# Kernel optimization log

Measured on AMD Instinct MI355X. Metric: run time of the kernel, lower is better.

## Reference

```python
import jax, jax.numpy as jnp
import numpy as np

B, T, C = 32, 128, 64
E, H = 8, 4            # feat_dim, num_heads
D = E // H             # head_dim = 2
HID = 32               # hidden_dim


def setup_inputs() -> dict:
    key = jax.random.key(0)
    ks = jax.random.split(key, 20)
    s = 0.1
    return {
        "x": jax.random.normal(ks[0], (B, T, C), jnp.float32),
        # input_proj: Linear(C, C)
        "W_in": jax.random.normal(ks[1], (C, C), jnp.float32) * s,
        "b_in": jax.random.normal(ks[2], (C,), jnp.float32) * s,
        # time_step_score: Linear(C, C//4) -> GELU -> Linear(C//4, 1) -> Sigmoid
        "W_ts1": jax.random.normal(ks[3], (C // 4, C), jnp.float32) * s,
        "b_ts1": jax.random.normal(ks[4], (C // 4,), jnp.float32) * s,
        "W_ts2": jax.random.normal(ks[5], (1, C // 4), jnp.float32) * s,
        "b_ts2": jax.random.normal(ks[6], (1,), jnp.float32) * s,
        # per-channel GRU(1 -> E): torch gate order (r, z, n)
        "W_ih": jax.random.normal(ks[7], (C, 3 * E), jnp.float32) * s,      # input size 1
        "W_hh": jax.random.normal(ks[8], (C, 3 * E, E), jnp.float32) * s,
        "b_ih": jax.random.normal(ks[9], (C, 3 * E), jnp.float32) * s,
        "b_hh": jax.random.normal(ks[10], (C, 3 * E), jnp.float32) * s,
        # shared MultiheadAttention(E, 4): packed in_proj + out_proj
        "W_qkv": jax.random.normal(ks[11], (3 * E, E), jnp.float32) * s,
        "b_qkv": jax.random.normal(ks[12], (3 * E,), jnp.float32) * s,
        "W_o": jax.random.normal(ks[13], (E, E), jnp.float32) * s,
        "b_o": jax.random.normal(ks[14], (E,), jnp.float32) * s,
        # out_proj: Linear(C*E, HID)
        "W_out": jax.random.normal(ks[15], (HID, C * E), jnp.float32) * s,
        "b_out": jax.random.normal(ks[16], (HID,), jnp.float32) * s,
    }


def _forward(x, W_in, b_in, W_ts1, b_ts1, W_ts2, b_ts2,
             W_ih, W_hh, b_ih, b_hh, W_qkv, b_qkv, W_o, b_o, W_out, b_out):
    bs, ts, c = x.shape
    # time step importance: per-timestep MLP over the raw features
    h1 = jax.nn.gelu(jnp.einsum('btc,fc->btf', x, W_ts1) + b_ts1, approximate=False)
    ts_imp = jax.nn.sigmoid(jnp.einsum('btf,of->bto', h1, W_ts2) + b_ts2)[..., 0]  # [B,T]

    xp = jnp.einsum('btc,dc->btd', x, W_in) + b_in  # [B,T,C]

    # Batched per-channel GRU scan over time. state h: [B,C,E]
    def step(h, x_t):
        gi = x_t[:, :, None] * W_ih[None] + b_ih          # [B,C,3E]
        gh = jnp.einsum('bce,cge->bcg', h, W_hh) + b_hh   # [B,C,3E]
        ir, iz, inn = gi[..., :E], gi[..., E:2 * E], gi[..., 2 * E:]
        hr, hz, hn = gh[..., :E], gh[..., E:2 * E], gh[..., 2 * E:]
        r = jax.nn.sigmoid(ir + hr)
        z = jax.nn.sigmoid(iz + hz)
        n = jnp.tanh(inn + r * hn)
        h_new = (1.0 - z) * n + z * h
        return h_new, h_new

    h0 = jnp.zeros((bs, c, E), xp.dtype)
    _, hs = jax.lax.scan(step, h0, jnp.transpose(xp, (1, 0, 2)))  # [T,B,C,E]
    hs_bcte = jnp.transpose(hs, (1, 2, 0, 3))                     # [B,C,T,E]

    # Shared MHA applied independently per channel (batched over B*C)
    qkv = jnp.einsum('bcte,fe->bctf', hs_bcte, W_qkv) + b_qkv     # [B,C,T,3E]
    q, k, v = qkv[..., :E], qkv[..., E:2 * E], qkv[..., 2 * E:]
    def heads(t):
        return t.reshape(bs, c, ts, H, D)
    q, k, v = heads(q), heads(k), heads(v)
    scores = jnp.einsum('bcthd,bcshd->bchts', q, k) / np.sqrt(D)
    attn = jax.nn.softmax(scores, axis=-1)
    o = jnp.einsum('bchts,bcshd->bcthd', attn, v).reshape(bs, c, ts, E)
    attn_out = jnp.einsum('bcte,fe->bctf', o, W_o) + b_o          # [B,C,T,E]
    attention = jnp.transpose(attn_out, (0, 2, 1, 3))             # [B,T,C,E]

    out_flat = jnp.transpose(hs, (1, 0, 2, 3)).reshape(bs, ts, c * E)  # [B,T,C*E]
    out = jnp.einsum('btf,hf->bth', out_flat, W_out) + b_out           # [B,T,HID]

    feat_imp = jax.nn.sigmoid(attention.sum(axis=(1, 3)))   # [B,C]
    tsf_imp = jax.nn.sigmoid(attention.sum(axis=-1))        # [B,T,C]
    return out[:, -1, :], feat_imp, ts_imp, tsf_imp


def reference(x, W_in, b_in, W_ts1, b_ts1, W_ts2, b_ts2,
              W_ih, W_hh, b_ih, b_hh, W_qkv, b_qkv, W_o, b_o, W_out, b_out):
    return _forward(x, W_in, b_in, W_ts1, b_ts1, W_ts2, b_ts2,
                    W_ih, W_hh, b_ih, b_hh, W_qkv, b_qkv, W_o, b_o, W_out, b_out)
```

## Files before the change

kernel.cpp:

```cpp
#include <hip/hip_runtime.h>
#include <hip/hip_bf16.h>
#include <math.h>

#define B_ 32
#define T_ 128
#define C_ 64
#define E_ 8
#define HID_ 32

#define LOG2E 1.44269504088896341f

__device__ __forceinline__ float fast_rcp(float x) { return __builtin_amdgcn_rcpf(x); }
__device__ __forceinline__ float fast_sigmoid(float x) {
    return fast_rcp(1.0f + exp2f(-LOG2E * x));
}
__device__ __forceinline__ float fast_tanh(float x) {
    float xc = __builtin_amdgcn_fmed3f(x, -15.0f, 15.0f);
    float t = exp2f(2.0f * LOG2E * xc);
    return (t - 1.0f) * fast_rcp(t + 1.0f);
}

__global__ __launch_bounds__(64) void k_gru(
    const float* __restrict__ x, const float* __restrict__ W_in, const float* __restrict__ b_in,
    const float* __restrict__ W_ih, const float* __restrict__ W_hh,
    const float* __restrict__ b_ih, const float* __restrict__ b_hh,
    float* __restrict__ hs, float* __restrict__ fh)
{
    const int tid = threadIdx.x;
    const int ci = tid >> 3;
    const int e = tid & 7;
    const int chain = blockIdx.x * 8 + ci;
    const int b = chain >> 6;
    const int c = chain & 63;

    __shared__ float wsh[8][C_];
    __shared__ float xc[8][T_ + 1];

#pragma unroll
    for (int i = 0; i < 8; ++i) {
        int idx = tid * 8 + i;
        int ci2 = idx >> 6;
        int cc = (blockIdx.x * 8 + ci2) & 63;
        wsh[ci2][idx & 63] = W_in[cc * C_ + (idx & 63)];
    }
    __syncthreads();

    const float bi = b_in[c];
    for (int tt = 0; tt < 16; ++tt) {
        const int t = e * 16 + tt;
        const float4* xr = (const float4*)(x + (b * T_ + t) * C_);
        float a = bi;
#pragma unroll
        for (int k4 = 0; k4 < 16; ++k4) {
            float4 xv = xr[k4];
            a = fmaf(xv.x, wsh[ci][k4 * 4 + 0], a);
            a = fmaf(xv.y, wsh[ci][k4 * 4 + 1], a);
            a = fmaf(xv.z, wsh[ci][k4 * 4 + 2], a);
            a = fmaf(xv.w, wsh[ci][k4 * 4 + 3], a);
        }
        xc[ci][t] = a;
    }
    __syncthreads();

    float wr[E_], wz[E_], wn[E_];
#pragma unroll
    for (int j = 0; j < E_; ++j) {
        wr[j] = W_hh[(c * 24 + 0 * E_ + e) * E_ + j];
        wz[j] = W_hh[(c * 24 + 1 * E_ + e) * E_ + j];
        wn[j] = W_hh[(c * 24 + 2 * E_ + e) * E_ + j];
    }
    const float wir = W_ih[c * 24 + e], wiz = W_ih[c * 24 + E_ + e], win = W_ih[c * 24 + 2 * E_ + e];
    const float cr = b_ih[c * 24 + e] + b_hh[c * 24 + e];
    const float cz = b_ih[c * 24 + E_ + e] + b_hh[c * 24 + E_ + e];
    const float bin_ = b_ih[c * 24 + 2 * E_ + e];
    const float bhn  = b_hh[c * 24 + 2 * E_ + e];

    float h = 0.0f;
    float xv = xc[ci][0];
    float* ho = hs + (size_t)chain * T_ * E_ + e;
    for (int t = 0; t < T_; ++t) {
        float xvn = xc[ci][t + 1];
        float hj0 = __shfl(h, 0, 8), hj1 = __shfl(h, 1, 8);
        float hj2 = __shfl(h, 2, 8), hj3 = __shfl(h, 3, 8);
        float hj4 = __shfl(h, 4, 8), hj5 = __shfl(h, 5, 8);
        float hj6 = __shfl(h, 6, 8), hj7 = __shfl(h, 7, 8);
        float grx = fmaf(xv, wir, cr);
        float gzx = fmaf(xv, wiz, cz);
        float gnx = fmaf(xv, win, bin_);
        float r0 = fmaf(hj1, wr[1], hj0 * wr[0]);
        float r1 = fmaf(hj3, wr[3], hj2 * wr[2]);
        float r2 = fmaf(hj5, wr[5], hj4 * wr[4]);
        float r3 = fmaf(hj7, wr[7], hj6 * wr[6]);
        float z0 = fmaf(hj1, wz[1], hj0 * wz[0]);
        float z1 = fmaf(hj3, wz[3], hj2 * wz[2]);
        float z2 = fmaf(hj5, wz[5], hj4 * wz[4]);
        float z3 = fmaf(hj7, wz[7], hj6 * wz[6]);
        float n0 = fmaf(hj1, wn[1], hj0 * wn[0]);
        float n1 = fmaf(hj3, wn[3], hj2 * wn[2]);
        float n2 = fmaf(hj5, wn[5], hj4 * wn[4]);
        float n3 = fmaf(hj7, wn[7], hj6 * wn[6]);
        float gr = grx + ((r0 + r1) + (r2 + r3));
        float gz = gzx + ((z0 + z1) + (z2 + z3));
        float hn = bhn + ((n0 + n1) + (n2 + n3));
        float r = fast_sigmoid(gr);
        float z = fast_sigmoid(gz);
        float nn = fast_tanh(fmaf(r, hn, gnx));
        h = fmaf(z, h - nn, nn);
        ho[t * E_] = h;
        xv = xvn;
    }
    fh[chain * E_ + e] = h;
}

__global__ __launch_bounds__(256) void k_attn(
    const float* __restrict__ hs, const float* __restrict__ W_qkv, const float* __restrict__ b_qkv,
    const float* __restrict__ W_o, const float* __restrict__ b_o,
    float* __restrict__ feat_imp, float* __restrict__ tsf_imp)
{
    const int bc = blockIdx.x;
    const int b = bc >> 6, c = bc & 63;
    const int tid = threadIdx.x;
    const int t2 = tid & 63;
    const int sq = tid >> 6;

    __shared__ __align__(16) float ks[T_][E_];
    __shared__ __align__(16) float us[T_][4];
    __shared__ float qsT[E_][T_];
    __shared__ float pacc[3][T_][8];
    __shared__ float red[T_];

    const float qscale = 0.70710678118654752f * LOG2E;

    {
        const int row = (tid < 128) ? tid : (tid - 128);
        const float4* hp = (const float4*)(hs + (size_t)bc * T_ * E_ + row * E_);
        float4 h0 = hp[0], h1 = hp[1];
        float hr[E_] = {h0.x, h0.y, h0.z, h0.w, h1.x, h1.y, h1.z, h1.w};
        if (tid < 128) {
            float kv[E_];
#pragma unroll
            for (int f = 0; f < E_; ++f) {
                float a = b_qkv[E_ + f];
#pragma unroll
                for (int j = 0; j < E_; ++j) a = fmaf(hr[j], W_qkv[(E_ + f) * E_ + j], a);
                kv[f] = a;
            }
            ((float4*)&ks[row][0])[0] = make_float4(kv[0], kv[1], kv[2], kv[3]);
            ((float4*)&ks[row][0])[1] = make_float4(kv[4], kv[5], kv[6], kv[7]);
#pragma unroll
            for (int f = 0; f < E_; ++f) {
                float a = b_qkv[f];
#pragma unroll
                for (int j = 0; j < E_; ++j) a = fmaf(hr[j], W_qkv[f * E_ + j], a);
                qsT[f][row] = a * qscale;
            }
        } else {
            float ws[E_];
#pragma unroll
            for (int d = 0; d < E_; ++d) {
                float w = 0.0f;
#pragma unroll
                for (int fp = 0; fp < E_; ++fp) w += W_o[fp * E_ + d];
                ws[d] = w;
            }
            float vv[E_];
#pragma unroll
            for (int f = 0; f < E_; ++f) {
                float a = b_qkv[2 * E_ + f];
#pragma unroll
                for (int j = 0; j < E_; ++j) a = fmaf(hr[j], W_qkv[(2 * E_ + f) * E_ + j], a);
                vv[f] = a;
            }
            float4 uu;
            uu.x = fmaf(vv[1], ws[1], vv[0] * ws[0]);
            uu.y = fmaf(vv[3], ws[3], vv[2] * ws[2]);
            uu.z = fmaf(vv[5], ws[5], vv[4] * ws[4]);
            uu.w = fmaf(vv[7], ws[7], vv[6] * ws[6]);
            *((float4*)&us[row][0]) = uu;
        }
    }
    __syncthreads();

    float q0[E_], q1[E_];
#pragma unroll
    for (int f = 0; f < E_; ++f) { q0[f] = qsT[f][t2]; q1[f] = qsT[f][t2 + 64]; }

    float l0[4] = {0.f,0.f,0.f,0.f}, S0[4] = {0.f,0.f,0.f,0.f};
    float l1[4] = {0.f,0.f,0.f,0.f}, S1[4] = {0.f,0.f,0.f,0.f};
    const float* kb = &ks[sq * 32][0];
    const float* ub = &us[sq * 32][0];
#pragma unroll 8
    for (int i = 0; i < 32; ++i) {
        float4 k0 = *(const float4*)(kb + i * 8);
        float4 k1 = *(const float4*)(kb + i * 8 + 4);
        float4 uu = *(const float4*)(ub + i * 4);
        float p00 = exp2f(fmaf(q0[1], k0.y, q0[0] * k0.x));
        float p01 = exp2f(fmaf(q0[3], k0.w, q0[2] * k0.z));
        float p02 = exp2f(fmaf(q0[5], k1.y, q0[4] * k1.x));
        float p03 = exp2f(fmaf(q0[7], k1.w, q0[6] * k1.z));
        float p10 = exp2f(fmaf(q1[1], k0.y, q1[0] * k0.x));
        float p11 = exp2f(fmaf(q1[3], k0.w, q1[2] * k0.z));
        float p12 = exp2f(fmaf(q1[5], k1.y, q1[4] * k1.x));
        float p13 = exp2f(fmaf(q1[7], k1.w, q1[6] * k1.z));
        l0[0] += p00; l0[1] += p01; l0[2] += p02; l0[3] += p03;
        l1[0] += p10; l1[1] += p11; l1[2] += p12; l1[3] += p13;
        S0[0] = fmaf(p00, uu.x, S0[0]); S0[1] = fmaf(p01, uu.y, S0[1]);
        S0[2] = fmaf(p02, uu.z, S0[2]); S0[3] = fmaf(p03, uu.w, S0[3]);
        S1[0] = fmaf(p10, uu.x, S1[0]); S1[1] = fmaf(p11, uu.y, S1[1]);
        S1[2] = fmaf(p12, uu.z, S1[2]); S1[3] = fmaf(p13, uu.w, S1[3]);
    }

    if (sq > 0) {
        float* pr = &pacc[sq - 1][t2][0];
#pragma unroll
        for (int i = 0; i < 4; ++i) { pr[i] = l0[i]; pr[4 + i] = S0[i]; }
        pr = &pacc[sq - 1][t2 + 64][0];
#pragma unroll
        for (int i = 0; i < 4; ++i) { pr[i] = l1[i]; pr[4 + i] = S1[i]; }
    }
    __syncthreads();

    if (sq == 0) {
        float bsum = 0.0f;
#pragma unroll
        for (int fp = 0; fp < E_; ++fp) bsum += b_o[fp];
#pragma unroll
        for (int qq = 0; qq < 3; ++qq) {
#pragma unroll
            for (int i = 0; i < 4; ++i) {
                l0[i] += pacc[qq][t2][i];       S0[i] += pacc[qq][t2][4 + i];
                l1[i] += pacc[qq][t2 + 64][i];  S1[i] += pacc[qq][t2 + 64][4 + i];
            }
        }
        float Sa = bsum, Sb = bsum;
#pragma unroll
        for (int hh = 0; hh < 4; ++hh) {
            Sa = fmaf(S0[hh], fast_rcp(l0[hh]), Sa);
            Sb = fmaf(S1[hh], fast_rcp(l1[hh]), Sb);
        }
        tsf_imp[(size_t)b * T_ * C_ + (size_t)t2 * C_ + c] = fast_sigmoid(Sa);
        tsf_imp[(size_t)b * T_ * C_ + (size_t)(t2 + 64) * C_ + c] = fast_sigmoid(Sb);
        red[t2] = Sa;
        red[t2 + 64] = Sb;
    }
    __syncthreads();
    for (int off = 64; off > 0; off >>= 1) {
        if (tid < off) red[tid] += red[tid + off];
        __syncthreads();
    }
    if (tid == 0) feat_imp[bc] = fast_sigmoid(red[0]);
}

__global__ __launch_bounds__(64) void k_ts(
    const float* __restrict__ x,
    const float* __restrict__ W_ts1, const float* __restrict__ b_ts1,
    const float* __restrict__ W_ts2, const float* __restrict__ b_ts2,
    float* __restrict__ ts_imp)
{
    const int bt = blockIdx.x;
    const int tid = threadIdx.x;
    __shared__ float xs[C_];
    __shared__ float h1[16];
    xs[tid] = x[bt * C_ + tid];
    __syncthreads();
    if (tid < 16) {
        float a = b_ts1[tid];
#pragma unroll
        for (int k = 0; k < C_; ++k) a = fmaf(xs[k], W_ts1[tid * C_ + k], a);
        h1[tid] = 0.5f * a * (1.0f + erff(a * 0.70710678118654752f));
    }
    __syncthreads();
    if (tid == 0) {
        float s = b_ts2[0];
#pragma unroll
        for (int k = 0; k < 16; ++k) s = fmaf(h1[k], W_ts2[k], s);
        ts_imp[bt] = fast_sigmoid(s);
    }
}

__global__ __launch_bounds__(64) void k_out(
    const float* __restrict__ fh, const float* __restrict__ W_out, const float* __restrict__ b_out,
    float* __restrict__ out0)
{
    const int b = blockIdx.x;
    const int tid = threadIdx.x;
    __shared__ float hf[C_ * E_];
    const float4* src = (const float4*)(fh + (b * C_ + tid) * E_);
    float4* dst = (float4*)(hf + tid * E_);
    dst[0] = src[0];
    dst[1] = src[1];
    __syncthreads();
    if (tid < HID_) {
        float a = b_out[tid];
        const float* wo = W_out + tid * (C_ * E_);
        for (int k = 0; k < C_ * E_; ++k) a = fmaf(hf[k], wo[k], a);
        out0[b * HID_ + tid] = a;
    }
}

extern "C" void kernel_launch(void* const* d_in, const int* in_sizes, int n_in,
                              void* d_out, int out_size, void* d_ws, size_t ws_size,
                              hipStream_t stream) {
    (void)in_sizes; (void)n_in; (void)out_size; (void)ws_size;

    float* out0 = (float*)d_out;
    float* feat = out0 + B_ * HID_;
    float* tsim = feat + B_ * C_;
    float* tsf  = tsim + B_ * T_;

    const float* x     = (const float*)d_in[0];
    const float* W_in  = (const float*)d_in[1];
    const float* b_in  = (const float*)d_in[2];
    const float* W_ts1 = (const float*)d_in[3];
    const float* b_ts1 = (const float*)d_in[4];
    const float* W_ts2 = (const float*)d_in[5];
    const float* b_ts2 = (const float*)d_in[6];
    const float* W_ih  = (const float*)d_in[7];
    const float* W_hh  = (const float*)d_in[8];
    const float* b_ih  = (const float*)d_in[9];
    const float* b_hh  = (const float*)d_in[10];
    const float* W_qkv = (const float*)d_in[11];
    const float* b_qkv = (const float*)d_in[12];
    const float* W_o   = (const float*)d_in[13];
    const float* b_o   = (const float*)d_in[14];
    const float* W_out = (const float*)d_in[15];
    const float* b_out = (const float*)d_in[16];

    float* fhb = (float*)d_ws;
    float* hsb = fhb + B_ * C_ * E_;

    hipLaunchKernelGGL(k_gru, dim3(B_ * C_ / 8), dim3(64), 0, stream,
                       x, W_in, b_in, W_ih, W_hh, b_ih, b_hh, hsb, fhb);
    hipLaunchKernelGGL(k_attn, dim3(B_ * C_), dim3(256), 0, stream,
                       hsb, W_qkv, b_qkv, W_o, b_o, feat, tsf);
    hipLaunchKernelGGL(k_ts, dim3(B_ * T_), dim3(64), 0, stream,
                       x, W_ts1, b_ts1, W_ts2, b_ts2, tsim);
    hipLaunchKernelGGL(k_out, dim3(B_), dim3(64), 0, stream,
                       fhb, W_out, b_out, out0);
}
```

Before: 93.19 us.

## Merge four kernels into two, stage GRU outputs in LDS, restructure attention reduction

Folds the time-step MLP into extra blocks of the GRU kernel and the final output projection into an extra block of the attention kernel, so the launch sequence shrinks from four kernels to two. GRU hidden states are buffered in shared memory and written back as coalesced float4 stores instead of strided scalar stores. The attention inner loop now gives each query row to a lane pair, which combine partial sums by shuffle, replacing the cross-wave LDS partial-accumulation pass and the tree reduction. Raw hardware exp2 builtins replace exp2f. The tradeoffs are a larger LDS footprint in the GRU kernel and a single output-projection block that may run as a serial tail.

```diff
diff --git a/kernel.cpp b/kernel.cpp
--- a/kernel.cpp
+++ b/kernel.cpp
@@ -11,30 +11,61 @@
 #define LOG2E 1.44269504088896341f
 
 __device__ __forceinline__ float fast_rcp(float x) { return __builtin_amdgcn_rcpf(x); }
+#if __has_builtin(__builtin_amdgcn_exp2f)
+__device__ __forceinline__ float fast_exp2(float x) { return __builtin_amdgcn_exp2f(x); }
+#else
+__device__ __forceinline__ float fast_exp2(float x) { return exp2f(x); }
+#endif
 __device__ __forceinline__ float fast_sigmoid(float x) {
-    return fast_rcp(1.0f + exp2f(-LOG2E * x));
+    return fast_rcp(1.0f + fast_exp2(-LOG2E * x));
 }
 __device__ __forceinline__ float fast_tanh(float x) {
     float xc = __builtin_amdgcn_fmed3f(x, -15.0f, 15.0f);
-    float t = exp2f(2.0f * LOG2E * xc);
+    float t = fast_exp2(2.0f * LOG2E * xc);
     return (t - 1.0f) * fast_rcp(t + 1.0f);
 }
 
-__global__ __launch_bounds__(64) void k_gru(
+__global__ __launch_bounds__(64) void k_gru_ts(
     const float* __restrict__ x, const float* __restrict__ W_in, const float* __restrict__ b_in,
     const float* __restrict__ W_ih, const float* __restrict__ W_hh,
     const float* __restrict__ b_ih, const float* __restrict__ b_hh,
-    float* __restrict__ hs, float* __restrict__ fh)
+    const float* __restrict__ W_ts1, const float* __restrict__ b_ts1,
+    const float* __restrict__ W_ts2, const float* __restrict__ b_ts2,
+    float* __restrict__ hs, float* __restrict__ fh, float* __restrict__ ts_imp)
 {
     const int tid = threadIdx.x;
+
+    __shared__ float wsh[8][C_];
+    __shared__ float xc[8][T_ + 1];
+    __shared__ float hsb[T_][68];
+
+    if (blockIdx.x >= 256) {
+        const int bt = blockIdx.x - 256;
+        float* xs = &wsh[0][0];
+        float* h1 = &xc[0][0];
+        xs[tid] = x[bt * C_ + tid];
+        __syncthreads();
+        if (tid < 16) {
+            float a = b_ts1[tid];
+#pragma unroll
+            for (int k = 0; k < C_; ++k) a = fmaf(xs[k], W_ts1[tid * C_ + k], a);
+            h1[tid] = 0.5f * a * (1.0f + erff(a * 0.70710678118654752f));
+        }
+        __syncthreads();
+        if (tid == 0) {
+            float s = b_ts2[0];
+#pragma unroll
+            for (int k = 0; k < 16; ++k) s = fmaf(h1[k], W_ts2[k], s);
+            ts_imp[bt] = fast_sigmoid(s);
+        }
+        return;
+    }
+
     const int ci = tid >> 3;
     const int e = tid & 7;
     const int chain = blockIdx.x * 8 + ci;
     const int b = chain >> 6;
     const int c = chain & 63;
-
-    __shared__ float wsh[8][C_];
-    __shared__ float xc[8][T_ + 1];
 
 #pragma unroll
     for (int i = 0; i < 8; ++i) {
@@ -77,7 +108,6 @@
 
     float h = 0.0f;
     float xv = xc[ci][0];
-    float* ho = hs + (size_t)chain * T_ * E_ + e;
     for (int t = 0; t < T_; ++t) {
         float xvn = xc[ci][t + 1];
         float hj0 = __shfl(h, 0, 8), hj1 = __shfl(h, 1, 8);
@@ -106,34 +136,68 @@
         float z = fast_sigmoid(gz);
         float nn = fast_tanh(fmaf(r, hn, gnx));
         h = fmaf(z, h - nn, nn);
-        ho[t * E_] = h;
+        hsb[t][tid] = h;
         xv = xvn;
     }
     fh[chain * E_ + e] = h;
-}
-
-__global__ __launch_bounds__(256) void k_attn(
+    __syncthreads();
+
+    float4* gdst = (float4*)(hs + (size_t)blockIdx.x * 8 * T_ * E_);
+#pragma unroll
+    for (int k = 0; k < 32; ++k) {
+        int idx4 = k * 64 + tid;
+        int fi = idx4 * 4;
+        int cc = fi >> 10;
+        int t = (fi >> 3) & 127;
+        int ee = fi & 7;
+        gdst[idx4] = *(const float4*)&hsb[t][cc * 8 + ee];
+    }
+}
+
+__global__ __launch_bounds__(256) void k_attn_out(
     const float* __restrict__ hs, const float* __restrict__ W_qkv, const float* __restrict__ b_qkv,
     const float* __restrict__ W_o, const float* __restrict__ b_o,
-    float* __restrict__ feat_imp, float* __restrict__ tsf_imp)
+    const float* __restrict__ fh, const float* __restrict__ W_out, const float* __restrict__ b_out,
+    float* __restrict__ out0, float* __restrict__ feat_imp, float* __restrict__ tsf_imp)
 {
+    const int tid = threadIdx.x;
+
+    if (blockIdx.x == B_ * C_) {
+#pragma unroll
+        for (int pi = tid; pi < B_ * HID_; pi += 256) {
+            int bb = pi >> 5, o = pi & 31;
+            const float4* hv = (const float4*)(fh + bb * C_ * E_);
+            const float4* wv = (const float4*)(W_out + o * C_ * E_);
+            float a = b_out[o];
+#pragma unroll 16
+            for (int k4 = 0; k4 < 128; ++k4) {
+                float4 h4 = hv[k4], w4 = wv[k4];
+                a = fmaf(h4.x, w4.x, a); a = fmaf(h4.y, w4.y, a);
+                a = fmaf(h4.z, w4.z, a); a = fmaf(h4.w, w4.w, a);
+            }
+            out0[pi] = a;
+        }
+        return;
+    }
+
     const int bc = blockIdx.x;
     const int b = bc >> 6, c = bc & 63;
-    const int tid = threadIdx.x;
-    const int t2 = tid & 63;
-    const int sq = tid >> 6;
+    const int w = tid >> 6;
+    const int lane = tid & 63;
+    const int ri = lane >> 1;
+    const int sh = lane & 1;
+    const int row = w * 32 + ri;
 
     __shared__ __align__(16) float ks[T_][E_];
     __shared__ __align__(16) float us[T_][4];
     __shared__ float qsT[E_][T_];
-    __shared__ float pacc[3][T_][8];
-    __shared__ float red[T_];
+    __shared__ float red4[4];
 
     const float qscale = 0.70710678118654752f * LOG2E;
 
     {
-        const int row = (tid < 128) ? tid : (tid - 128);
-        const float4* hp = (const float4*)(hs + (size_t)bc * T_ * E_ + row * E_);
+        const int srow = (tid < 128) ? tid : (tid - 128);
+        const float4* hp = (const float4*)(hs + (size_t)bc * T_ * E_ + srow * E_);
         float4 h0 = hp[0], h1 = hp[1];
         float hr[E_] = {h0.x, h0.y, h0.z, h0.w, h1.x, h1.y, h1.z, h1.w};
         if (tid < 128) {
@@ -145,23 +209,23 @@
                 for (int j = 0; j < E_; ++j) a = fmaf(hr[j], W_qkv[(E_ + f) * E_ + j], a);
                 kv[f] = a;
             }
-            ((float4*)&ks[row][0])[0] = make_float4(kv[0], kv[1], kv[2], kv[3]);
-            ((float4*)&ks[row][0])[1] = make_float4(kv[4], kv[5], kv[6], kv[7]);
+            ((float4*)&ks[srow][0])[0] = make_float4(kv[0], kv[1], kv[2], kv[3]);
+            ((float4*)&ks[srow][0])[1] = make_float4(kv[4], kv[5], kv[6], kv[7]);
 #pragma unroll
             for (int f = 0; f < E_; ++f) {
                 float a = b_qkv[f];
 #pragma unroll
                 for (int j = 0; j < E_; ++j) a = fmaf(hr[j], W_qkv[f * E_ + j], a);
-                qsT[f][row] = a * qscale;
+                qsT[f][srow] = a * qscale;
             }
         } else {
             float ws[E_];
 #pragma unroll
             for (int d = 0; d < E_; ++d) {
-                float w = 0.0f;
-#pragma unroll
-                for (int fp = 0; fp < E_; ++fp) w += W_o[fp * E_ + d];
-                ws[d] = w;
+                float wv = 0.0f;
+#pragma unroll
+                for (int fp = 0; fp < E_; ++fp) wv += W_o[fp * E_ + d];
+                ws[d] = wv;
             }
             float vv[E_];
 #pragma unroll
@@ -176,126 +240,58 @@
             uu.y = fmaf(vv[3], ws[3], vv[2] * ws[2]);
             uu.z = fmaf(vv[5], ws[5], vv[4] * ws[4]);
             uu.w = fmaf(vv[7], ws[7], vv[6] * ws[6]);
-            *((float4*)&us[row][0]) = uu;
-        }
-    }
-    __syncthreads();
-
-    float q0[E_], q1[E_];
-#pragma unroll
-    for (int f = 0; f < E_; ++f) { q0[f] = qsT[f][t2]; q1[f] = qsT[f][t2 + 64]; }
-
-    float l0[4] = {0.f,0.f,0.f,0.f}, S0[4] = {0.f,0.f,0.f,0.f};
-    float l1[4] = {0.f,0.f,0.f,0.f}, S1[4] = {0.f,0.f,0.f,0.f};
-    const float* kb = &ks[sq * 32][0];
-    const float* ub = &us[sq * 32][0];
+            *((float4*)&us[srow][0]) = uu;
+        }
+    }
+    __syncthreads();
+
+    float q[E_];
+#pragma unroll
+    for (int f = 0; f < E_; ++f) q[f] = qsT[f][row];
+
+    float l[4] = {0.f, 0.f, 0.f, 0.f};
+    float S[4] = {0.f, 0.f, 0.f, 0.f};
+    const float* kb = &ks[sh * 64][0];
+    const float* ub = &us[sh * 64][0];
 #pragma unroll 8
-    for (int i = 0; i < 32; ++i) {
+    for (int i = 0; i < 64; ++i) {
         float4 k0 = *(const float4*)(kb + i * 8);
         float4 k1 = *(const float4*)(kb + i * 8 + 4);
         float4 uu = *(const float4*)(ub + i * 4);
-        float p00 = exp2f(fmaf(q0[1], k0.y, q0[0] * k0.x));
-        float p01 = exp2f(fmaf(q0[3], k0.w, q0[2] * k0.z));
-        float p02 = exp2f(fmaf(q0[5], k1.y, q0[4] * k1.x));
-        float p03 = exp2f(fmaf(q0[7], k1.w, q0[6] * k1.z));
-        float p10 = exp2f(fmaf(q1[1], k0.y, q1[0] * k0.x));
-        float p11 = exp2f(fmaf(q1[3], k0.w, q1[2] * k0.z));
-        float p12 = exp2f(fmaf(q1[5], k1.y, q1[4] * k1.x));
-        float p13 = exp2f(fmaf(q1[7], k1.w, q1[6] * k1.z));
-        l0[0] += p00; l0[1] += p01; l0[2] += p02; l0[3] += p03;
-        l1[0] += p10; l1[1] += p11; l1[2] += p12; l1[3] += p13;
-        S0[0] = fmaf(p00, uu.x, S0[0]); S0[1] = fmaf(p01, uu.y, S0[1]);
-        S0[2] = fmaf(p02, uu.z, S0[2]); S0[3] = fmaf(p03, uu.w, S0[3]);
-        S1[0] = fmaf(p10, uu.x, S1[0]); S1[1] = fmaf(p11, uu.y, S1[1]);
-        S1[2] = fmaf(p12, uu.z, S1[2]); S1[3] = fmaf(p13, uu.w, S1[3]);
-    }
-
-    if (sq > 0) {
-        float* pr = &pacc[sq - 1][t2][0];
-#pragma unroll
-        for (int i = 0; i < 4; ++i) { pr[i] = l0[i]; pr[4 + i] = S0[i]; }
-        pr = &pacc[sq - 1][t2 + 64][0];
-#pragma unroll
-        for (int i = 0; i < 4; ++i) { pr[i] = l1[i]; pr[4 + i] = S1[i]; }
-    }
-    __syncthreads();
-
-    if (sq == 0) {
-        float bsum = 0.0f;
-#pragma unroll
-        for (int fp = 0; fp < E_; ++fp) bsum += b_o[fp];
-#pragma unroll
-        for (int qq = 0; qq < 3; ++qq) {
-#pragma unroll
-            for (int i = 0; i < 4; ++i) {
-                l0[i] += pacc[qq][t2][i];       S0[i] += pacc[qq][t2][4 + i];
-                l1[i] += pacc[qq][t2 + 64][i];  S1[i] += pacc[qq][t2 + 64][4 + i];
-            }
-        }
-        float Sa = bsum, Sb = bsum;
-#pragma unroll
-        for (int hh = 0; hh < 4; ++hh) {
-            Sa = fmaf(S0[hh], fast_rcp(l0[hh]), Sa);
-            Sb = fmaf(S1[hh], fast_rcp(l1[hh]), Sb);
-        }
-        tsf_imp[(size_t)b * T_ * C_ + (size_t)t2 * C_ + c] = fast_sigmoid(Sa);
-        tsf_imp[(size_t)b * T_ * C_ + (size_t)(t2 + 64) * C_ + c] = fast_sigmoid(Sb);
-        red[t2] = Sa;
-        red[t2 + 64] = Sb;
-    }
-    __syncthreads();
-    for (int off = 64; off > 0; off >>= 1) {
-        if (tid < off) red[tid] += red[tid + off];
-        __syncthreads();
-    }
-    if (tid == 0) feat_imp[bc] = fast_sigmoid(red[0]);
-}
-
-__global__ __launch_bounds__(64) void k_ts(
-    const float* __restrict__ x,
-    const float* __restrict__ W_ts1, const float* __restrict__ b_ts1,
-    const float* __restrict__ W_ts2, const float* __restrict__ b_ts2,
-    float* __restrict__ ts_imp)
-{
-    const int bt = blockIdx.x;
-    const int tid = threadIdx.x;
-    __shared__ float xs[C_];
-    __shared__ float h1[16];
-    xs[tid] = x[bt * C_ + tid];
-    __syncthreads();
-    if (tid < 16) {
-        float a = b_ts1[tid];
-#pragma unroll
-        for (int k = 0; k < C_; ++k) a = fmaf(xs[k], W_ts1[tid * C_ + k], a);
-        h1[tid] = 0.5f * a * (1.0f + erff(a * 0.70710678118654752f));
-    }
-    __syncthreads();
-    if (tid == 0) {
-        float s = b_ts2[0];
-#pragma unroll
-        for (int k = 0; k < 16; ++k) s = fmaf(h1[k], W_ts2[k], s);
-        ts_imp[bt] = fast_sigmoid(s);
-    }
-}
-
-__global__ __launch_bounds__(64) void k_out(
-    const float* __restrict__ fh, const float* __restrict__ W_out, const float* __restrict__ b_out,
-    float* __restrict__ out0)
-{
-    const int b = blockIdx.x;
-    const int tid = threadIdx.x;
-    __shared__ float hf[C_ * E_];
-    const float4* src = (const float4*)(fh + (b * C_ + tid) * E_);
-    float4* dst = (float4*)(hf + tid * E_);
-    dst[0] = src[0];
-    dst[1] = src[1];
-    __syncthreads();
-    if (tid < HID_) {
-        float a = b_out[tid];
-        const float* wo = W_out + tid * (C_ * E_);
-        for (int k = 0; k < C_ * E_; ++k) a = fmaf(hf[k], wo[k], a);
-        out0[b * HID_ + tid] = a;
-    }
+        float p0 = fast_exp2(fmaf(q[1], k0.y, q[0] * k0.x));
+        float p1 = fast_exp2(fmaf(q[3], k0.w, q[2] * k0.z));
+        float p2 = fast_exp2(fmaf(q[5], k1.y, q[4] * k1.x));
+        float p3 = fast_exp2(fmaf(q[7], k1.w, q[6] * k1.z));
+        l[0] += p0; l[1] += p1; l[2] += p2; l[3] += p3;
+        S[0] = fmaf(p0, uu.x, S[0]);
+        S[1] = fmaf(p1, uu.y, S[1]);
+        S[2] = fmaf(p2, uu.z, S[2]);
+        S[3] = fmaf(p3, uu.w, S[3]);
+    }
+
+#pragma unroll
+    for (int i = 0; i < 4; ++i) {
+        l[i] += __shfl_xor(l[i], 1);
+        S[i] += __shfl_xor(S[i], 1);
+    }
+
+    float bsum = 0.0f;
+#pragma unroll
+    for (int fp = 0; fp < E_; ++fp) bsum += b_o[fp];
+    float Sv = bsum;
+#pragma unroll
+    for (int hh = 0; hh < 4; ++hh) Sv = fmaf(S[hh], fast_rcp(l[hh]), Sv);
+
+    if (sh == 0)
+        tsf_imp[(size_t)b * T_ * C_ + (size_t)row * C_ + c] = fast_sigmoid(Sv);
+
+    float fsum = Sv;
+#pragma unroll
+    for (int off = 2; off <= 32; off <<= 1) fsum += __shfl_xor(fsum, off);
+    if (lane == 0) red4[w] = fsum;
+    __syncthreads();
+    if (tid == 0)
+        feat_imp[bc] = fast_sigmoid(red4[0] + red4[1] + red4[2] + red4[3]);
 }
 
 extern "C" void kernel_launch(void* const* d_in, const int* in_sizes, int n_in,
@@ -329,12 +325,10 @@
     float* fhb = (float*)d_ws;
     float* hsb = fhb + B_ * C_ * E_;
 
-    hipLaunchKernelGGL(k_gru, dim3(B_ * C_ / 8), dim3(64), 0, stream,
-                       x, W_in, b_in, W_ih, W_hh, b_ih, b_hh, hsb, fhb);
-    hipLaunchKernelGGL(k_attn, dim3(B_ * C_), dim3(256), 0, stream,
-                       hsb, W_qkv, b_qkv, W_o, b_o, feat, tsf);
-    hipLaunchKernelGGL(k_ts, dim3(B_ * T_), dim3(64), 0, stream,
-                       x, W_ts1, b_ts1, W_ts2, b_ts2, tsim);
-    hipLaunchKernelGGL(k_out, dim3(B_), dim3(64), 0, stream,
-                       fhb, W_out, b_out, out0);
-}
+    hipLaunchKernelGGL(k_gru_ts, dim3(256 + B_ * T_), dim3(64), 0, stream,
+                       x, W_in, b_in, W_ih, W_hh, b_ih, b_hh,
+                       W_ts1, b_ts1, W_ts2, b_ts2, hsb, fhb, tsim);
+    hipLaunchKernelGGL(k_attn_out, dim3(B_ * C_ + 1), dim3(256), 0, stream,
+                       hsb, W_qkv, b_qkv, W_o, b_o,
+                       fhb, W_out, b_out, out0, feat, tsf);
+}
```

Measured after the change: 126.7 us. +35.9%, slower.

## Split input projection into separate kernel and give each GRU thread two hidden units

Applied to the files above, without the earlier changes.

Moves the input projection out of the GRU kernel into a new k_pre kernel that writes xp to workspace, so the GRU kernel only loads precomputed values into shared memory. The GRU is remapped from 8 threads per chain (one hidden unit each) to 4 threads per chain (two units each), which replaces the 8 broadcast shuffles with a few xor shuffles and permuted weights, and packs 16 chains into each block. This aims to shorten the serial recurrence step and cut the redundant projection work done in every GRU block. The cost is an extra kernel launch, a global round-trip for xp, and half as many GRU blocks, which lowers parallelism.

```diff
diff --git a/kernel.cpp b/kernel.cpp
--- a/kernel.cpp
+++ b/kernel.cpp
@@ -11,105 +11,124 @@
 #define LOG2E 1.44269504088896341f
 
 __device__ __forceinline__ float fast_rcp(float x) { return __builtin_amdgcn_rcpf(x); }
+__device__ __forceinline__ float fast_exp2(float x) { return exp2f(x); }
 __device__ __forceinline__ float fast_sigmoid(float x) {
-    return fast_rcp(1.0f + exp2f(-LOG2E * x));
+    return fast_rcp(1.0f + fast_exp2(-LOG2E * x));
 }
 __device__ __forceinline__ float fast_tanh(float x) {
     float xc = __builtin_amdgcn_fmed3f(x, -15.0f, 15.0f);
-    float t = exp2f(2.0f * LOG2E * xc);
+    float t = fast_exp2(2.0f * LOG2E * xc);
     return (t - 1.0f) * fast_rcp(t + 1.0f);
 }
 
+__global__ __launch_bounds__(64) void k_pre(
+    const float* __restrict__ x, const float* __restrict__ W_in, const float* __restrict__ b_in,
+    float* __restrict__ xp)
+{
+    const int bt = blockIdx.x;
+    const int tid = threadIdx.x;
+    __shared__ __align__(16) float4 xs4[16];
+    if (tid < 16) xs4[tid] = ((const float4*)(x + bt * C_))[tid];
+    __syncthreads();
+    float a = b_in[tid];
+    const float4* w4 = (const float4*)(W_in + tid * C_);
+#pragma unroll
+    for (int k4 = 0; k4 < 16; ++k4) {
+        float4 xv = xs4[k4];
+        float4 wv = w4[k4];
+        a = fmaf(xv.x, wv.x, a); a = fmaf(xv.y, wv.y, a);
+        a = fmaf(xv.z, wv.z, a); a = fmaf(xv.w, wv.w, a);
+    }
+    xp[bt * C_ + tid] = a;
+}
+
 __global__ __launch_bounds__(64) void k_gru(
-    const float* __restrict__ x, const float* __restrict__ W_in, const float* __restrict__ b_in,
-    const float* __restrict__ W_ih, const float* __restrict__ W_hh,
+    const float* __restrict__ xp, const float* __restrict__ W_ih, const float* __restrict__ W_hh,
     const float* __restrict__ b_ih, const float* __restrict__ b_hh,
     float* __restrict__ hs, float* __restrict__ fh)
 {
     const int tid = threadIdx.x;
-    const int ci = tid >> 3;
-    const int e = tid & 7;
-    const int chain = blockIdx.x * 8 + ci;
-    const int b = chain >> 6;
+    const int ci = tid >> 2;
+    const int q  = tid & 3;
+    const int chain = blockIdx.x * 16 + ci;
     const int c = chain & 63;
 
-    __shared__ float wsh[8][C_];
-    __shared__ float xc[8][T_ + 1];
-
-#pragma unroll
-    for (int i = 0; i < 8; ++i) {
-        int idx = tid * 8 + i;
-        int ci2 = idx >> 6;
-        int cc = (blockIdx.x * 8 + ci2) & 63;
-        wsh[ci2][idx & 63] = W_in[cc * C_ + (idx & 63)];
-    }
-    __syncthreads();
-
-    const float bi = b_in[c];
-    for (int tt = 0; tt < 16; ++tt) {
-        const int t = e * 16 + tt;
-        const float4* xr = (const float4*)(x + (b * T_ + t) * C_);
-        float a = bi;
-#pragma unroll
-        for (int k4 = 0; k4 < 16; ++k4) {
-            float4 xv = xr[k4];
-            a = fmaf(xv.x, wsh[ci][k4 * 4 + 0], a);
-            a = fmaf(xv.y, wsh[ci][k4 * 4 + 1], a);
-            a = fmaf(xv.z, wsh[ci][k4 * 4 + 2], a);
-            a = fmaf(xv.w, wsh[ci][k4 * 4 + 3], a);
-        }
-        xc[ci][t] = a;
-    }
-    __syncthreads();
-
-    float wr[E_], wz[E_], wn[E_];
-#pragma unroll
-    for (int j = 0; j < E_; ++j) {
-        wr[j] = W_hh[(c * 24 + 0 * E_ + e) * E_ + j];
-        wz[j] = W_hh[(c * 24 + 1 * E_ + e) * E_ + j];
-        wn[j] = W_hh[(c * 24 + 2 * E_ + e) * E_ + j];
-    }
-    const float wir = W_ih[c * 24 + e], wiz = W_ih[c * 24 + E_ + e], win = W_ih[c * 24 + 2 * E_ + e];
-    const float cr = b_ih[c * 24 + e] + b_hh[c * 24 + e];
-    const float cz = b_ih[c * 24 + E_ + e] + b_hh[c * 24 + E_ + e];
-    const float bin_ = b_ih[c * 24 + 2 * E_ + e];
-    const float bhn  = b_hh[c * 24 + 2 * E_ + e];
-
-    float h = 0.0f;
+    __shared__ float xc[16][T_ + 1];
+
+    const int c_base = (blockIdx.x & 3) * 16;
+    const int bb = blockIdx.x >> 2;
+    for (int idx = tid; idx < 16 * T_; idx += 64) {
+        int cci = idx & 15;
+        int t = idx >> 4;
+        xc[cci][t] = xp[(bb * T_ + t) * C_ + c_base + cci];
+    }
+    __syncthreads();
+
+    float wr[2][8], wz[2][8], wn[2][8];
+    float wir[2], wiz[2], win_[2], cr[2], cz[2], bin_[2], bhn[2];
+#pragma unroll
+    for (int u = 0; u < 2; ++u) {
+        const int e = 2 * q + u;
+#pragma unroll
+        for (int m = 0; m < 4; ++m) {
+#pragma unroll
+            for (int p = 0; p < 2; ++p) {
+                const int j = 2 * (q ^ m) + p;
+                wr[u][2 * m + p] = W_hh[(c * 24 + 0  + e) * 8 + j];
+                wz[u][2 * m + p] = W_hh[(c * 24 + 8  + e) * 8 + j];
+                wn[u][2 * m + p] = W_hh[(c * 24 + 16 + e) * 8 + j];
+            }
+        }
+        wir[u] = W_ih[c * 24 + e];
+        wiz[u] = W_ih[c * 24 + 8 + e];
+        win_[u] = W_ih[c * 24 + 16 + e];
+        cr[u] = b_ih[c * 24 + e] + b_hh[c * 24 + e];
+        cz[u] = b_ih[c * 24 + 8 + e] + b_hh[c * 24 + 8 + e];
+        bin_[u] = b_ih[c * 24 + 16 + e];
+        bhn[u]  = b_hh[c * 24 + 16 + e];
+    }
+
+    float ha = 0.0f, hb = 0.0f;
+    float* hop = hs + (size_t)chain * T_ * E_ + 2 * q;
     float xv = xc[ci][0];
-    float* ho = hs + (size_t)chain * T_ * E_ + e;
     for (int t = 0; t < T_; ++t) {
         float xvn = xc[ci][t + 1];
-        float hj0 = __shfl(h, 0, 8), hj1 = __shfl(h, 1, 8);
-        float hj2 = __shfl(h, 2, 8), hj3 = __shfl(h, 3, 8);
-        float hj4 = __shfl(h, 4, 8), hj5 = __shfl(h, 5, 8);
-        float hj6 = __shfl(h, 6, 8), hj7 = __shfl(h, 7, 8);
-        float grx = fmaf(xv, wir, cr);
-        float gzx = fmaf(xv, wiz, cz);
-        float gnx = fmaf(xv, win, bin_);
-        float r0 = fmaf(hj1, wr[1], hj0 * wr[0]);
-        float r1 = fmaf(hj3, wr[3], hj2 * wr[2]);
-        float r2 = fmaf(hj5, wr[5], hj4 * wr[4]);
-        float r3 = fmaf(hj7, wr[7], hj6 * wr[6]);
-        float z0 = fmaf(hj1, wz[1], hj0 * wz[0]);
-        float z1 = fmaf(hj3, wz[3], hj2 * wz[2]);
-        float z2 = fmaf(hj5, wz[5], hj4 * wz[4]);
-        float z3 = fmaf(hj7, wz[7], hj6 * wz[6]);
-        float n0 = fmaf(hj1, wn[1], hj0 * wn[0]);
-        float n1 = fmaf(hj3, wn[3], hj2 * wn[2]);
-        float n2 = fmaf(hj5, wn[5], hj4 * wn[4]);
-        float n3 = fmaf(hj7, wn[7], hj6 * wn[6]);
-        float gr = grx + ((r0 + r1) + (r2 + r3));
-        float gz = gzx + ((z0 + z1) + (z2 + z3));
-        float hn = bhn + ((n0 + n1) + (n2 + n3));
-        float r = fast_sigmoid(gr);
-        float z = fast_sigmoid(gz);
-        float nn = fast_tanh(fmaf(r, hn, gnx));
-        h = fmaf(z, h - nn, nn);
-        ho[t * E_] = h;
+        float pa1 = __shfl_xor(ha, 1), pb1 = __shfl_xor(hb, 1);
+        float pa2 = __shfl_xor(ha, 2), pb2 = __shfl_xor(hb, 2);
+        float pa3 = __shfl_xor(pa1, 2), pb3 = __shfl_xor(pb1, 2);
+        const float pa[4] = {ha, pa1, pa2, pa3};
+        const float pb[4] = {hb, pb1, pb2, pb3};
+        float hnew[2];
+#pragma unroll
+        for (int u = 0; u < 2; ++u) {
+            float g0 = fmaf(pb[0], wr[u][1], pa[0] * wr[u][0]);
+            float g1 = fmaf(pb[1], wr[u][3], pa[1] * wr[u][2]);
+            float g2 = fmaf(pb[2], wr[u][5], pa[2] * wr[u][4]);
+            float g3 = fmaf(pb[3], wr[u][7], pa[3] * wr[u][6]);
+            float gr = fmaf(xv, wir[u], cr[u]) + ((g0 + g1) + (g2 + g3));
+            float z0 = fmaf(pb[0], wz[u][1], pa[0] * wz[u][0]);
+            float z1 = fmaf(pb[1], wz[u][3], pa[1] * wz[u][2]);
+            float z2 = fmaf(pb[2], wz[u][5], pa[2] * wz[u][4]);
+            float z3 = fmaf(pb[3], wz[u][7], pa[3] * wz[u][6]);
+            float gz = fmaf(xv, wiz[u], cz[u]) + ((z0 + z1) + (z2 + z3));
+            float n0 = fmaf(pb[0], wn[u][1], pa[0] * wn[u][0]);
+            float n1 = fmaf(pb[1], wn[u][3], pa[1] * wn[u][2]);
+            float n2 = fmaf(pb[2], wn[u][5], pa[2] * wn[u][4]);
+            float n3 = fmaf(pb[3], wn[u][7], pa[3] * wn[u][6]);
+            float hn = bhn[u] + ((n0 + n1) + (n2 + n3));
+            float gn = fmaf(xv, win_[u], bin_[u]);
+            float r = fast_sigmoid(gr);
+            float z = fast_sigmoid(gz);
+            float nn = fast_tanh(fmaf(r, hn, gn));
+            float hu = (u == 0) ? ha : hb;
+            hnew[u] = fmaf(z, hu - nn, nn);
+        }
+        ha = hnew[0]; hb = hnew[1];
+        *(float2*)(hop + (size_t)t * E_) = make_float2(ha, hb);
         xv = xvn;
     }
-    fh[chain * E_ + e] = h;
+    fh[chain * E_ + 2 * q] = ha;
+    fh[chain * E_ + 2 * q + 1] = hb;
 }
 
 __global__ __launch_bounds__(256) void k_attn(
@@ -158,10 +177,10 @@
             float ws[E_];
 #pragma unroll
             for (int d = 0; d < E_; ++d) {
-                float w = 0.0f;
-#pragma unroll
-                for (int fp = 0; fp < E_; ++fp) w += W_o[fp * E_ + d];
-                ws[d] = w;
+                float wv = 0.0f;
+#pragma unroll
+                for (int fp = 0; fp < E_; ++fp) wv += W_o[fp * E_ + d];
+                ws[d] = wv;
             }
             float vv[E_];
 #pragma unroll
@@ -194,14 +213,14 @@
         float4 k0 = *(const float4*)(kb + i * 8);
         float4 k1 = *(const float4*)(kb + i * 8 + 4);
         float4 uu = *(const float4*)(ub + i * 4);
-        float p00 = exp2f(fmaf(q0[1], k0.y, q0[0] * k0.x));
-        float p01 = exp2f(fmaf(q0[3], k0.w, q0[2] * k0.z));
-        float p02 = exp2f(fmaf(q0[5], k1.y, q0[4] * k1.x));
-        float p03 = exp2f(fmaf(q0[7], k1.w, q0[6] * k1.z));
-        float p10 = exp2f(fmaf(q1[1], k0.y, q1[0] * k0.x));
-        float p11 = exp2f(fmaf(q1[3], k0.w, q1[2] * k0.z));
-        float p12 = exp2f(fmaf(q1[5], k1.y, q1[4] * k1.x));
-        float p13 = exp2f(fmaf(q1[7], k1.w, q1[6] * k1.z));
+        float p00 = fast_exp2(fmaf(q0[1], k0.y, q0[0] * k0.x));
+        float p01 = fast_exp2(fmaf(q0[3], k0.w, q0[2] * k0.z));
+        float p02 = fast_exp2(fmaf(q0[5], k1.y, q0[4] * k1.x));
+        float p03 = fast_exp2(fmaf(q0[7], k1.w, q0[6] * k1.z));
+        float p10 = fast_exp2(fmaf(q1[1], k0.y, q1[0] * k0.x));
+        float p11 = fast_exp2(fmaf(q1[3], k0.w, q1[2] * k0.z));
+        float p12 = fast_exp2(fmaf(q1[5], k1.y, q1[4] * k1.x));
+        float p13 = fast_exp2(fmaf(q1[7], k1.w, q1[6] * k1.z));
         l0[0] += p00; l0[1] += p01; l0[2] += p02; l0[3] += p03;
         l1[0] += p10; l1[1] += p11; l1[2] += p12; l1[3] += p13;
         S0[0] = fmaf(p00, uu.x, S0[0]); S0[1] = fmaf(p01, uu.y, S0[1]);
@@ -327,10 +346,12 @@
     const float* b_out = (const float*)d_in[16];
 
     float* fhb = (float*)d_ws;
-    float* hsb = fhb + B_ * C_ * E_;
-
-    hipLaunchKernelGGL(k_gru, dim3(B_ * C_ / 8), dim3(64), 0, stream,
-                       x, W_in, b_in, W_ih, W_hh, b_ih, b_hh, hsb, fhb);
+    float* xpb = fhb + B_ * C_ * E_;
+    float* hsb = xpb + (size_t)B_ * T_ * C_;
+
+    hipLaunchKernelGGL(k_pre, dim3(B_ * T_), dim3(64), 0, stream, x, W_in, b_in, xpb);
+    hipLaunchKernelGGL(k_gru, dim3(B_ * C_ / 16), dim3(64), 0, stream,
+                       xpb, W_ih, W_hh, b_ih, b_hh, hsb, fhb);
     hipLaunchKernelGGL(k_attn, dim3(B_ * C_), dim3(256), 0, stream,
                        hsb, W_qkv, b_qkv, W_o, b_o, feat, tsf);
     hipLaunchKernelGGL(k_ts, dim3(B_ * T_), dim3(64), 0, stream,
```

Result: slower. 111.1 us (+19.2%).
